# Optimization experiments

Hardware: AMD Instinct MI355X
Metric: run time of the kernel (lower is better)

## Reference

```python
import jax, jax.numpy as jnp
import numpy as np

POSE, Z, H, E = 62, 32, 256, 6

def setup_inputs() -> dict:
    key = jax.random.key(0)
    ks = jax.random.split(key, 32)
    it = iter(ks)
    def W(o, i):
        return (jax.random.normal(next(it), (o, i), jnp.float32) * 0.05)
    def B(o):
        return jnp.zeros((o,), jnp.float32)
    def WE(o, i):
        return (jax.random.normal(next(it), (E, o, i), jnp.float32) * 0.05)
    def BE(o):
        return jnp.zeros((E, o), jnp.float32)
    d = {}
    d['prev_pose'] = jax.random.normal(next(it), (POSE,), jnp.float32)
    d['curr_pose'] = jax.random.normal(next(it), (POSE,), jnp.float32)
    d['eps'] = jax.random.normal(next(it), (Z,), jnp.float32)
    # encoder
    d['enc_w0'], d['enc_b0'] = W(H, POSE + POSE), B(H)
    d['enc_w1'], d['enc_b1'] = W(H, H), B(H)
    d['enc_w2'], d['enc_b2'] = W(H, H), B(H)
    d['mu_w'], d['mu_b'] = W(Z, H), B(Z)
    d['lv_w'], d['lv_b'] = W(Z, H), B(Z)
    # gating network
    d['gate_w0'], d['gate_b0'] = W(H, Z + POSE), B(H)
    d['gate_w1'], d['gate_b1'] = W(H, H), B(H)
    d['gate_w2'], d['gate_b2'] = W(H, H), B(H)
    d['gate_w3'], d['gate_b3'] = W(E, H), B(E)
    # 6 experts, stacked on leading expert axis
    d['exp_w0'], d['exp_b0'] = WE(H, Z + POSE), BE(H)
    d['exp_w1'], d['exp_b1'] = WE(H, Z + H), BE(H)
    d['exp_w2'], d['exp_b2'] = WE(H, Z + H), BE(H)
    d['exp_w3'], d['exp_b3'] = WE(POSE, Z + H), BE(POSE)
    return d

def _forward(prev_pose, curr_pose, eps,
             enc_w0, enc_b0, enc_w1, enc_b1, enc_w2, enc_b2,
             mu_w, mu_b, lv_w, lv_b,
             gate_w0, gate_b0, gate_w1, gate_b1, gate_w2, gate_b2,
             gate_w3, gate_b3,
             exp_w0, exp_b0, exp_w1, exp_b1, exp_w2, exp_b2,
             exp_w3, exp_b3):
    elu = jax.nn.elu
    # encode
    x = elu(enc_w0 @ jnp.concatenate([prev_pose, curr_pose]) + enc_b0)
    x = elu(enc_w1 @ x + enc_b1)
    x = elu(enc_w2 @ x + enc_b2)
    mu = mu_w @ x + mu_b
    logvar = lv_w @ x + lv_b
    # reparameterize (eps supplied as input for determinism)
    z = mu + eps * jnp.exp(0.5 * logvar)
    # gating network (raw logits, no softmax -- as in the original)
    g_in = jnp.concatenate([z, prev_pose])  # [94]
    g = elu(gate_w0 @ g_in + gate_b0)
    g = elu(gate_w1 @ g + gate_b1)
    g = elu(gate_w2 @ g + gate_b2)
    gates = gate_w3 @ g + gate_b3  # [6]
    # all 6 experts batched along leading axis e
    z_e = jnp.broadcast_to(z, (E, Z))  # [6,32]
    h = elu(jnp.einsum('eoh,h->eo', exp_w0, g_in) + exp_b0)       # [6,256]
    h = elu(jnp.einsum('eoh,eh->eo', exp_w1,
                       jnp.concatenate([z_e, h], axis=1)) + exp_b1)
    h = elu(jnp.einsum('eoh,eh->eo', exp_w2,
                       jnp.concatenate([z_e, h], axis=1)) + exp_b2)
    out_e = jnp.einsum('eoh,eh->eo', exp_w3,
                       jnp.concatenate([z_e, h], axis=1)) + exp_b3  # [6,62]
    decoded = jnp.sum(out_e * gates[:, None], axis=0)  # [62]
    return decoded, mu, logvar

def reference(prev_pose, curr_pose, eps,
              enc_w0, enc_b0, enc_w1, enc_b1, enc_w2, enc_b2,
              mu_w, mu_b, lv_w, lv_b,
              gate_w0, gate_b0, gate_w1, gate_b1, gate_w2, gate_b2,
              gate_w3, gate_b3,
              exp_w0, exp_b0, exp_w1, exp_b1, exp_w2, exp_b2,
              exp_w3, exp_b3):
    return _forward(prev_pose, curr_pose, eps,
                    enc_w0, enc_b0, enc_w1, enc_b1, enc_w2, enc_b2,
                    mu_w, mu_b, lv_w, lv_b,
                    gate_w0, gate_b0, gate_w1, gate_b1, gate_w2, gate_b2,
                    gate_w3, gate_b3,
                    exp_w0, exp_b0, exp_w1, exp_b1, exp_w2, exp_b2,
                    exp_w3, exp_b3)
```

## Files before the change

kernel.cpp:

```cpp
#include <hip/hip_runtime.h>
#include <math.h>


#define NWG   64
#define BLOCK 256

__device__ __align__(128) float g_a0[256];
__device__ __align__(128) float g_a1[256];
__device__ __align__(128) float g_a2[256];
__device__ __align__(128) float g_mu[32];
__device__ __align__(128) float g_lv[32];
__device__ __align__(128) float g_g0[256];
__device__ __align__(128) float g_g1[256];
__device__ __align__(128) float g_g2[256];
__device__ __align__(128) float g_gates[32];
__device__ __align__(128) float g_h0[1536];
__device__ __align__(128) float g_h1[1536];
__device__ __align__(128) float g_h2[1536];
__device__ __align__(128) float g_oute[384];

struct P {
  const float *prev, *curr, *eps;
  const float *ew0,*eb0,*ew1,*eb1,*ew2,*eb2;
  const float *muw,*mub,*lvw,*lvb;
  const float *gw0,*gb0,*gw1,*gb1,*gw2,*gb2,*gw3,*gb3;
  const float *xw0,*xb0,*xw1,*xb1,*xw2,*xb2,*xw3,*xb3;
  float* out;
};

__device__ __forceinline__ float cload(const float* a) {
  int v = __hip_atomic_load((const int*)a, __ATOMIC_RELAXED,
                            __HIP_MEMORY_SCOPE_AGENT);
  return __int_as_float(v);
}
__device__ __forceinline__ void cstore(float* a, float v) {
  __hip_atomic_store((int*)a, __float_as_int(v), __ATOMIC_RELAXED,
                     __HIP_MEMORY_SCOPE_AGENT);
}

__device__ __forceinline__ void gll16(const void* g, void* l) {
  __builtin_amdgcn_global_load_lds((const __attribute__((address_space(1))) void*)g,
                                   (__attribute__((address_space(3))) void*)l,
                                   16, 0, 0);
}
__device__ __forceinline__ void gll4(const void* g, void* l) {
  __builtin_amdgcn_global_load_lds((const __attribute__((address_space(1))) void*)g,
                                   (__attribute__((address_space(3))) void*)l,
                                   4, 0, 0);
}

__device__ __forceinline__ float wred(float v) {
#pragma unroll
  for (int m = 32; m; m >>= 1) v += __shfl_xor(v, m, 64);
  return v;
}
__device__ __forceinline__ float elu(float x) { return x > 0.f ? x : expm1f(x); }
__device__ __forceinline__ float dot4(float4 a, float4 b) {
  return a.x*b.x + a.y*b.y + a.z*b.z + a.w*b.w;
}

__device__ __forceinline__ void gridbar(int* flags, int phase) {
  __syncthreads();
  if (threadIdx.x == 0)
    __hip_atomic_store(&flags[blockIdx.x * 16], phase,
                       __ATOMIC_RELAXED, __HIP_MEMORY_SCOPE_AGENT);
  if (threadIdx.x < NWG) {
    while (__hip_atomic_load(&flags[threadIdx.x * 16],
                             __ATOMIC_RELAXED, __HIP_MEMORY_SCOPE_AGENT) < phase)
      __builtin_amdgcn_s_sleep(1);
  }
  __syncthreads();
}

__device__ __forceinline__ void copy_act(const float* gg, const float* gh,
                                         float* sg, float* sh,
                                         int wvin, int lane) {
  if (wvin == 0) { gll16(gh +        lane*4, sh);
                   gll16(gh + 1024 + lane*4, sh + 1024); }
  if (wvin == 1) { gll16(gh +  256 + lane*4, sh +  256);
                   gll16(gh + 1280 + lane*4, sh + 1280); }
  if (wvin == 2) { gll16(gh +  512 + lane*4, sh +  512);
                   gll16(gg +        lane*4, sg); }
  if (wvin == 3) { gll16(gh +  768 + lane*4, sh +  768); }
}

__global__ __launch_bounds__(BLOCK, 1) void mvae_main(P p, int* flags) {
  const int tid  = threadIdx.x;
  const int lane = tid & 63;
  const int wvin = tid >> 6;
  const int W    = blockIdx.x * 4 + wvin;

  __shared__ __align__(16) float s_w1[4][256];
  __shared__ __align__(16) float s_w2[4][256];
  __shared__ __align__(16) float s_w3[4][256];
  __shared__ __align__(16) float s_w4[4][7][96];
  __shared__ __align__(16) float s_w5[4][7][288];
  __shared__ __align__(16) float s_w6[4][7][288];
  __shared__ __align__(16) float s_w7[4][2][288];
  __shared__ __align__(16) float s_g[256];
  __shared__ __align__(16) float s_h[1536];
  __shared__ __align__(16) float s_a[256];
  __shared__ float s_z[32];
  __shared__ float s_gg[8];
  __shared__ float s_o[384];

  const float* w0r = p.ew0 + W * 124;
  float w0a = w0r[lane];
  float w0b = (lane < 60) ? w0r[64 + lane] : 0.f;
  float x0a = (lane < 62) ? p.prev[lane] : p.curr[lane - 62];
  float x0b = (lane < 60) ? p.curr[lane + 2] : 0.f;
  float prevA = (lane >= 32) ? p.prev[lane - 32] : 0.f;
  float prevB = (lane < 30) ? p.prev[32 + lane] : 0.f;
  float epsv  = (tid < 32) ? p.eps[tid] : 0.f;

  gll16(p.ew1 + W * 256 + lane * 4, s_w1[wvin]);
  gll16(p.ew2 + W * 256 + lane * 4, s_w2[wvin]);
  if (blockIdx.x < 16) {
    const float* src = (W < 32) ? p.muw + W * 256 : p.lvw + (W - 32) * 256;
    gll16(src + lane * 4, s_w3[wvin]);
  }
#pragma unroll
  for (int k = 0; k < 7; ++k) {
    int r = W + 256 * k;
    const float* src = (r < 256) ? p.gw0 + r * 94 : p.xw0 + (r - 256) * 94;
    float* dst = s_w4[wvin][k];
    if (lane < 23)       gll16(src + lane * 4, dst);
    else if (lane == 23) { gll4(src + 92, dst + 69);
                           gll4(src + 93, dst + 70); }
  }
#pragma unroll
  for (int k = 0; k < 7; ++k) {
    int r = W + 256 * k;
    float* dst = s_w5[wvin][k];
    if (r < 256) gll16(p.gw1 + r * 256 + lane * 4, dst);
    else {
      const float* src = p.xw1 + (r - 256) * 288;
      gll16(src + lane * 4, dst);
      if (lane < 8) gll16(src + 256 + lane * 4, dst + 256);
    }
  }
#pragma unroll
  for (int k = 0; k < 7; ++k) {
    int r = W + 256 * k;
    float* dst = s_w6[wvin][k];
    if (r < 256) gll16(p.gw2 + r * 256 + lane * 4, dst);
    else {
      const float* src = p.xw2 + (r - 256) * 288;
      gll16(src + lane * 4, dst);
      if (lane < 8) gll16(src + 256 + lane * 4, dst + 256);
    }
  }
  {
    float* dst = s_w7[wvin][0];
    if (W < 6) gll16(p.gw3 + W * 256 + lane * 4, dst);
    else {
      const float* src = p.xw3 + (W - 6) * 288;
      gll16(src + lane * 4, dst);
      if (lane < 8) gll16(src + 256 + lane * 4, dst + 256);
    }
  }
  if (W < 122) {
    float* dst = s_w7[wvin][1];
    const float* src = p.xw3 + (W + 250) * 288;
    gll16(src + lane * 4, dst);
    if (lane < 8) gll16(src + 256 + lane * 4, dst + 256);
  }

  {
    float s = wred(w0a * x0a + w0b * x0b);
    if (!lane) cstore(&g_a0[W], elu(s + p.eb0[W]));
  }
  gridbar(flags, 1);

  if (wvin == 0) gll16((const float*)g_a0 + lane * 4, s_a);
  __syncthreads();
  {
    float4 w = *(const float4*)(s_w1[wvin] + 4 * lane);
    float4 x = *(const float4*)(s_a + 4 * lane);
    float s = wred(dot4(w, x));
    if (!lane) cstore(&g_a1[W], elu(s + p.eb1[W]));
  }
  gridbar(flags, 2);

  if (wvin == 0) gll16((const float*)g_a1 + lane * 4, s_a);
  __syncthreads();
  {
    float4 w = *(const float4*)(s_w2[wvin] + 4 * lane);
    float4 x = *(const float4*)(s_a + 4 * lane);
    float s = wred(dot4(w, x));
    if (!lane) cstore(&g_a2[W], elu(s + p.eb2[W]));
  }
  gridbar(flags, 3);

  if (blockIdx.x < 16) {
    if (wvin == 0) gll16((const float*)g_a2 + lane * 4, s_a);
    __syncthreads();
    float4 w = *(const float4*)(s_w3[wvin] + 4 * lane);
    float4 x = *(const float4*)(s_a + 4 * lane);
    float s = wred(dot4(w, x));
    if (!lane) {
      if (W < 32) { float v = s + p.mub[W]; cstore(&g_mu[W], v); p.out[62 + W] = v; }
      else { int r = W - 32; float v = s + p.lvb[r]; cstore(&g_lv[r], v); p.out[94 + r] = v; }
    }
  }
  gridbar(flags, 4);

  if (tid < 32)
    s_z[tid] = cload(&g_mu[tid]) + epsv * expf(0.5f * cload(&g_lv[tid]));
  __syncthreads();

  {
    float xa = (lane < 32) ? s_z[lane] : prevA;
#pragma unroll
    for (int k = 0; k < 7; ++k) {
      int r = W + 256 * k;
      const float* wrow = s_w4[wvin][k];
      float wb = (lane < 30) ? wrow[64 + lane] : 0.f;
      float s = wred(wrow[lane] * xa + wb * prevB);
      if (!lane) {
        if (r < 256) cstore(&g_g0[r], elu(s + p.gb0[r]));
        else         cstore(&g_h0[r - 256], elu(s + p.xb0[r - 256]));
      }
    }
  }
  gridbar(flags, 5);

  copy_act(g_g0, g_h0, s_g, s_h, wvin, lane);
  __syncthreads();
#pragma unroll
  for (int k = 0; k < 7; ++k) {
    int r = W + 256 * k;
    const float* wrow = s_w5[wvin][k];
    float4 w = *(const float4*)(wrow + 4 * lane);
    if (r < 256) {
      float4 x = *(const float4*)(s_g + 4 * lane);
      float s = wred(dot4(w, x));
      if (!lane) cstore(&g_g1[r], elu(s + p.gb1[r]));
    } else {
      int q = r - 256, e = q >> 8;
      float4 xh;
      if (lane < 8) xh = *(const float4*)(s_z + 4 * lane);
      else          xh = *(const float4*)(s_h + e * 256 + 4 * lane - 32);
      float s = dot4(w, xh);
      if (lane < 32) s += wrow[256 + lane] * s_h[e * 256 + 224 + lane];
      s = wred(s);
      if (!lane) cstore(&g_h1[q], elu(s + p.xb1[q]));
    }
  }
  gridbar(flags, 6);

  copy_act(g_g1, g_h1, s_g, s_h, wvin, lane);
  __syncthreads();
#pragma unroll
  for (int k = 0; k < 7; ++k) {
    int r = W + 256 * k;
    const float* wrow = s_w6[wvin][k];
    float4 w = *(const float4*)(wrow + 4 * lane);
    if (r < 256) {
      float4 x = *(const float4*)(s_g + 4 * lane);
      float s = wred(dot4(w, x));
      if (!lane) cstore(&g_g2[r], elu(s + p.gb2[r]));
    } else {
      int q = r - 256, e = q >> 8;
      float4 xh;
      if (lane < 8) xh = *(const float4*)(s_z + 4 * lane);
      else          xh = *(const float4*)(s_h + e * 256 + 4 * lane - 32);
      float s = dot4(w, xh);
      if (lane < 32) s += wrow[256 + lane] * s_h[e * 256 + 224 + lane];
      s = wred(s);
      if (!lane) cstore(&g_h2[q], elu(s + p.xb2[q]));
    }
  }
  gridbar(flags, 7);

  copy_act(g_g2, g_h2, s_g, s_h, wvin, lane);
  __syncthreads();
  {
    const float* wrow = s_w7[wvin][0];
    float4 w = *(const float4*)(wrow + 4 * lane);
    if (W < 6) {
      float4 x = *(const float4*)(s_g + 4 * lane);
      float s = wred(dot4(w, x));
      if (!lane) cstore(&g_gates[W], s + p.gb3[W]);
    } else {
      int q = W - 6, e = q / 62;
      float4 xh;
      if (lane < 8) xh = *(const float4*)(s_z + 4 * lane);
      else          xh = *(const float4*)(s_h + e * 256 + 4 * lane - 32);
      float s = dot4(w, xh);
      if (lane < 32) s += wrow[256 + lane] * s_h[e * 256 + 224 + lane];
      s = wred(s);
      if (!lane) cstore(&g_oute[q], s + p.xb3[q]);
    }
  }
  if (W < 122) {
    const float* wrow = s_w7[wvin][1];
    float4 w = *(const float4*)(wrow + 4 * lane);
    int q = W + 250, e = q / 62;
    float4 xh;
    if (lane < 8) xh = *(const float4*)(s_z + 4 * lane);
    else          xh = *(const float4*)(s_h + e * 256 + 4 * lane - 32);
    float s = dot4(w, xh);
    if (lane < 32) s += wrow[256 + lane] * s_h[e * 256 + 224 + lane];
    s = wred(s);
    if (!lane) cstore(&g_oute[q], s + p.xb3[q]);
  }
  gridbar(flags, 8);

  if (blockIdx.x == 0) {
    s_o[tid] = cload(&g_oute[tid]);
    if (tid < 116) s_o[tid + 256] = cload(&g_oute[tid + 256]);
    if (tid < 6)   s_gg[tid] = cload(&g_gates[tid]);
    __syncthreads();
    if (tid < 62) {
      float s = 0.f;
#pragma unroll
      for (int e = 0; e < 6; ++e) s += s_o[e * 62 + tid] * s_gg[e];
      p.out[tid] = s;
    }
  }
}

extern "C" void kernel_launch(void* const* d_in, const int* in_sizes, int n_in,
                              void* d_out, int out_size, void* d_ws, size_t ws_size,
                              hipStream_t stream) {
  (void)in_sizes; (void)n_in; (void)out_size; (void)ws_size;
  const float* const* in = (const float* const*)d_in;
  P p;
  p.prev = in[0];  p.curr = in[1];  p.eps = in[2];
  p.ew0 = in[3];   p.eb0 = in[4];   p.ew1 = in[5];  p.eb1 = in[6];
  p.ew2 = in[7];   p.eb2 = in[8];
  p.muw = in[9];   p.mub = in[10];  p.lvw = in[11]; p.lvb = in[12];
  p.gw0 = in[13];  p.gb0 = in[14];  p.gw1 = in[15]; p.gb1 = in[16];
  p.gw2 = in[17];  p.gb2 = in[18];  p.gw3 = in[19]; p.gb3 = in[20];
  p.xw0 = in[21];  p.xb0 = in[22];  p.xw1 = in[23]; p.xb1 = in[24];
  p.xw2 = in[25];  p.xb2 = in[26];  p.xw3 = in[27]; p.xb3 = in[28];
  p.out = (float*)d_out;

  int* flags = (int*)d_ws;
  hipMemsetAsync(flags, 0, NWG * 16 * sizeof(int), stream);
  mvae_main<<<NWG, BLOCK, 0, stream>>>(p, flags);
}
```

Baseline: 39.99 us.

## Compute encoder redundantly per workgroup to remove four grid barriers

Every workgroup now computes the full encoder (three 256-wide layers plus mu/logvar) on its own, reading the weights straight from global/L2 into shared-memory activations. This replaces the distributed encoder, which needed four grid-wide barriers and global activation exchanges. The cost is 64x redundant encoder work and weight traffic (about 0.6 MB per block, mostly L2 hits), done as serial per-wave loops of 64 rows, in exchange for cutting the number of grid barriers from eight to four.

New measurement: 114.9 us. 187% more time.

```diff
diff --git a/kernel.cpp b/kernel.cpp
--- a/kernel.cpp
+++ b/kernel.cpp
@@ -5,11 +5,6 @@
 #define NWG   64
 #define BLOCK 256
 
-__device__ __align__(128) float g_a0[256];
-__device__ __align__(128) float g_a1[256];
-__device__ __align__(128) float g_a2[256];
-__device__ __align__(128) float g_mu[32];
-__device__ __align__(128) float g_lv[32];
 __device__ __align__(128) float g_g0[256];
 __device__ __align__(128) float g_g1[256];
 __device__ __align__(128) float g_g2[256];
@@ -90,35 +85,24 @@
   const int wvin = tid >> 6;
   const int W    = blockIdx.x * 4 + wvin;
 
-  __shared__ __align__(16) float s_w1[4][256];
-  __shared__ __align__(16) float s_w2[4][256];
-  __shared__ __align__(16) float s_w3[4][256];
   __shared__ __align__(16) float s_w4[4][7][96];
   __shared__ __align__(16) float s_w5[4][7][288];
   __shared__ __align__(16) float s_w6[4][7][288];
   __shared__ __align__(16) float s_w7[4][2][288];
   __shared__ __align__(16) float s_g[256];
   __shared__ __align__(16) float s_h[1536];
-  __shared__ __align__(16) float s_a[256];
-  __shared__ float s_z[32];
+  __shared__ __align__(16) float s_x[128];
+  __shared__ __align__(16) float s_a0[256];
+  __shared__ __align__(16) float s_a1[256];
+  __shared__ __align__(16) float s_a2[256];
+  __shared__ __align__(16) float s_zp[96];
+  __shared__ float s_ml[64];
+  __shared__ float s_o[384];
   __shared__ float s_gg[8];
-  __shared__ float s_o[384];
-
-  const float* w0r = p.ew0 + W * 124;
-  float w0a = w0r[lane];
-  float w0b = (lane < 60) ? w0r[64 + lane] : 0.f;
-  float x0a = (lane < 62) ? p.prev[lane] : p.curr[lane - 62];
-  float x0b = (lane < 60) ? p.curr[lane + 2] : 0.f;
-  float prevA = (lane >= 32) ? p.prev[lane - 32] : 0.f;
-  float prevB = (lane < 30) ? p.prev[32 + lane] : 0.f;
-  float epsv  = (tid < 32) ? p.eps[tid] : 0.f;
-
-  gll16(p.ew1 + W * 256 + lane * 4, s_w1[wvin]);
-  gll16(p.ew2 + W * 256 + lane * 4, s_w2[wvin]);
-  if (blockIdx.x < 16) {
-    const float* src = (W < 32) ? p.muw + W * 256 : p.lvw + (W - 32) * 256;
-    gll16(src + lane * 4, s_w3[wvin]);
-  }
+
+  if (tid < 124) s_x[tid] = (tid < 62) ? p.prev[tid] : p.curr[tid - 62];
+  if (tid < 62)  s_zp[32 + tid] = p.prev[tid];
+
 #pragma unroll
   for (int k = 0; k < 7; ++k) {
     int r = W + 256 * k;
@@ -166,112 +150,134 @@
     if (lane < 8) gll16(src + 256 + lane * 4, dst + 256);
   }
 
-  {
-    float s = wred(w0a * x0a + w0b * x0b);
-    if (!lane) cstore(&g_a0[W], elu(s + p.eb0[W]));
-  }
-  gridbar(flags, 1);
-
-  if (wvin == 0) gll16((const float*)g_a0 + lane * 4, s_a);
-  __syncthreads();
-  {
-    float4 w = *(const float4*)(s_w1[wvin] + 4 * lane);
-    float4 x = *(const float4*)(s_a + 4 * lane);
-    float s = wred(dot4(w, x));
-    if (!lane) cstore(&g_a1[W], elu(s + p.eb1[W]));
-  }
-  gridbar(flags, 2);
-
-  if (wvin == 0) gll16((const float*)g_a1 + lane * 4, s_a);
-  __syncthreads();
-  {
-    float4 w = *(const float4*)(s_w2[wvin] + 4 * lane);
-    float4 x = *(const float4*)(s_a + 4 * lane);
-    float s = wred(dot4(w, x));
-    if (!lane) cstore(&g_a2[W], elu(s + p.eb2[W]));
-  }
-  gridbar(flags, 3);
-
-  if (blockIdx.x < 16) {
-    if (wvin == 0) gll16((const float*)g_a2 + lane * 4, s_a);
-    __syncthreads();
-    float4 w = *(const float4*)(s_w3[wvin] + 4 * lane);
-    float4 x = *(const float4*)(s_a + 4 * lane);
-    float s = wred(dot4(w, x));
-    if (!lane) {
-      if (W < 32) { float v = s + p.mub[W]; cstore(&g_mu[W], v); p.out[62 + W] = v; }
-      else { int r = W - 32; float v = s + p.lvb[r]; cstore(&g_lv[r], v); p.out[94 + r] = v; }
-    }
-  }
-  gridbar(flags, 4);
-
-  if (tid < 32)
-    s_z[tid] = cload(&g_mu[tid]) + epsv * expf(0.5f * cload(&g_lv[tid]));
-  __syncthreads();
-
-  {
-    float xa = (lane < 32) ? s_z[lane] : prevA;
+  __syncthreads();
+
+  {
+    float4 x0 = make_float4(0.f, 0.f, 0.f, 0.f);
+    if (lane < 31) x0 = *(const float4*)(s_x + 4 * lane);
+    for (int i = 0; i < 64; ++i) {
+      int r = (wvin << 6) | i;
+      float4 w = make_float4(0.f, 0.f, 0.f, 0.f);
+      if (lane < 31) w = *(const float4*)(p.ew0 + r * 124 + 4 * lane);
+      float s = wred(dot4(w, x0));
+      if (!lane) s_a0[r] = elu(s + p.eb0[r]);
+    }
+  }
+  __syncthreads();
+
+  {
+    float4 x = *(const float4*)(s_a0 + 4 * lane);
+    for (int i = 0; i < 64; ++i) {
+      int r = (wvin << 6) | i;
+      float4 w = *(const float4*)(p.ew1 + r * 256 + 4 * lane);
+      float s = wred(dot4(w, x));
+      if (!lane) s_a1[r] = elu(s + p.eb1[r]);
+    }
+  }
+  __syncthreads();
+
+  {
+    float4 x = *(const float4*)(s_a1 + 4 * lane);
+    for (int i = 0; i < 64; ++i) {
+      int r = (wvin << 6) | i;
+      float4 w = *(const float4*)(p.ew2 + r * 256 + 4 * lane);
+      float s = wred(dot4(w, x));
+      if (!lane) s_a2[r] = elu(s + p.eb2[r]);
+    }
+  }
+  __syncthreads();
+
+  {
+    float4 x = *(const float4*)(s_a2 + 4 * lane);
+    for (int i = 0; i < 16; ++i) {
+      int row = (wvin << 4) | i;
+      const float* wr = (row < 32) ? p.muw + row * 256
+                                   : p.lvw + (row - 32) * 256;
+      float4 w = *(const float4*)(wr + 4 * lane);
+      float s = wred(dot4(w, x));
+      if (!lane)
+        s_ml[row] = s + ((row < 32) ? p.mub[row] : p.lvb[row - 32]);
+    }
+  }
+  __syncthreads();
+
+  if (tid < 32) {
+    float mu = s_ml[tid], lv = s_ml[32 + tid];
+    s_zp[tid] = mu + p.eps[tid] * expf(0.5f * lv);
+    if (blockIdx.x == 0) { p.out[62 + tid] = mu; p.out[94 + tid] = lv; }
+  }
+  __syncthreads();
+
+  {
+    float xa = s_zp[lane];
+    float xb = (lane < 30) ? s_zp[64 + lane] : 0.f;
 #pragma unroll
     for (int k = 0; k < 7; ++k) {
       int r = W + 256 * k;
       const float* wrow = s_w4[wvin][k];
       float wb = (lane < 30) ? wrow[64 + lane] : 0.f;
-      float s = wred(wrow[lane] * xa + wb * prevB);
+      float s = wred(wrow[lane] * xa + wb * xb);
       if (!lane) {
         if (r < 256) cstore(&g_g0[r], elu(s + p.gb0[r]));
         else         cstore(&g_h0[r - 256], elu(s + p.xb0[r - 256]));
       }
     }
   }
-  gridbar(flags, 5);
+  gridbar(flags, 1);
 
   copy_act(g_g0, g_h0, s_g, s_h, wvin, lane);
   __syncthreads();
-#pragma unroll
-  for (int k = 0; k < 7; ++k) {
-    int r = W + 256 * k;
-    const float* wrow = s_w5[wvin][k];
-    float4 w = *(const float4*)(wrow + 4 * lane);
-    if (r < 256) {
-      float4 x = *(const float4*)(s_g + 4 * lane);
-      float s = wred(dot4(w, x));
-      if (!lane) cstore(&g_g1[r], elu(s + p.gb1[r]));
-    } else {
-      int q = r - 256, e = q >> 8;
-      float4 xh;
-      if (lane < 8) xh = *(const float4*)(s_z + 4 * lane);
-      else          xh = *(const float4*)(s_h + e * 256 + 4 * lane - 32);
-      float s = dot4(w, xh);
-      if (lane < 32) s += wrow[256 + lane] * s_h[e * 256 + 224 + lane];
-      s = wred(s);
-      if (!lane) cstore(&g_h1[q], elu(s + p.xb1[q]));
-    }
-  }
-  gridbar(flags, 6);
+  {
+    float4 xg = *(const float4*)(s_g + 4 * lane);
+    float4 xz4 = make_float4(0.f, 0.f, 0.f, 0.f);
+    if (lane < 8) xz4 = *(const float4*)(s_zp + 4 * lane);
+#pragma unroll
+    for (int k = 0; k < 7; ++k) {
+      int r = W + 256 * k;
+      const float* wrow = s_w5[wvin][k];
+      float4 w = *(const float4*)(wrow + 4 * lane);
+      if (r < 256) {
+        float s = wred(dot4(w, xg));
+        if (!lane) cstore(&g_g1[r], elu(s + p.gb1[r]));
+      } else {
+        int q = r - 256, e = q >> 8;
+        float4 xh = xz4;
+        if (lane >= 8) xh = *(const float4*)(s_h + e * 256 + 4 * lane - 32);
+        float s = dot4(w, xh);
+        if (lane < 32) s += wrow[256 + lane] * s_h[e * 256 + 224 + lane];
+        s = wred(s);
+        if (!lane) cstore(&g_h1[q], elu(s + p.xb1[q]));
+      }
+    }
+  }
+  gridbar(flags, 2);
 
   copy_act(g_g1, g_h1, s_g, s_h, wvin, lane);
   __syncthreads();
-#pragma unroll
-  for (int k = 0; k < 7; ++k) {
-    int r = W + 256 * k;
-    const float* wrow = s_w6[wvin][k];
-    float4 w = *(const float4*)(wrow + 4 * lane);
-    if (r < 256) {
-      float4 x = *(const float4*)(s_g + 4 * lane);
-      float s = wred(dot4(w, x));
-      if (!lane) cstore(&g_g2[r], elu(s + p.gb2[r]));
-    } else {
-      int q = r - 256, e = q >> 8;
-      float4 xh;
-      if (lane < 8) xh = *(const float4*)(s_z + 4 * lane);
-      else          xh = *(const float4*)(s_h + e * 256 + 4 * lane - 32);
-      float s = dot4(w, xh);
-      if (lane < 32) s += wrow[256 + lane] * s_h[e * 256 + 224 + lane];
-      s = wred(s);
-      if (!lane) cstore(&g_h2[q], elu(s + p.xb2[q]));
-    }
-  }
-  gridbar(flags, 7);
+  {
+    float4 xg = *(const float4*)(s_g + 4 * lane);
+    float4 xz4 = make_float4(0.f, 0.f, 0.f, 0.f);
+    if (lane < 8) xz4 = *(const float4*)(s_zp + 4 * lane);
+#pragma unroll
+    for (int k = 0; k < 7; ++k) {
+      int r = W + 256 * k;
+      const float* wrow = s_w6[wvin][k];
+      float4 w = *(const float4*)(wrow + 4 * lane);
+      if (r < 256) {
+        float s = wred(dot4(w, xg));
+        if (!lane) cstore(&g_g2[r], elu(s + p.gb2[r]));
+      } else {
+        int q = r - 256, e = q >> 8;
+        float4 xh = xz4;
+        if (lane >= 8) xh = *(const float4*)(s_h + e * 256 + 4 * lane - 32);
+        float s = dot4(w, xh);
+        if (lane < 32) s += wrow[256 + lane] * s_h[e * 256 + 224 + lane];
+        s = wred(s);
+        if (!lane) cstore(&g_h2[q], elu(s + p.xb2[q]));
+      }
+    }
+  }
+  gridbar(flags, 3);
 
   copy_act(g_g2, g_h2, s_g, s_h, wvin, lane);
   __syncthreads();
@@ -284,8 +290,8 @@
       if (!lane) cstore(&g_gates[W], s + p.gb3[W]);
     } else {
       int q = W - 6, e = q / 62;
-      float4 xh;
-      if (lane < 8) xh = *(const float4*)(s_z + 4 * lane);
+      float4 xh = make_float4(0.f, 0.f, 0.f, 0.f);
+      if (lane < 8) xh = *(const float4*)(s_zp + 4 * lane);
       else          xh = *(const float4*)(s_h + e * 256 + 4 * lane - 32);
       float s = dot4(w, xh);
       if (lane < 32) s += wrow[256 + lane] * s_h[e * 256 + 224 + lane];
@@ -297,15 +303,15 @@
     const float* wrow = s_w7[wvin][1];
     float4 w = *(const float4*)(wrow + 4 * lane);
     int q = W + 250, e = q / 62;
-    float4 xh;
-    if (lane < 8) xh = *(const float4*)(s_z + 4 * lane);
+    float4 xh = make_float4(0.f, 0.f, 0.f, 0.f);
+    if (lane < 8) xh = *(const float4*)(s_zp + 4 * lane);
     else          xh = *(const float4*)(s_h + e * 256 + 4 * lane - 32);
     float s = dot4(w, xh);
     if (lane < 32) s += wrow[256 + lane] * s_h[e * 256 + 224 + lane];
     s = wred(s);
     if (!lane) cstore(&g_oute[q], s + p.xb3[q]);
   }
-  gridbar(flags, 8);
+  gridbar(flags, 4);
 
   if (blockIdx.x == 0) {
     s_o[tid] = cload(&g_oute[tid]);
```
